# Performance work log

Measured on AMD Instinct MI355X. Metric: run time of the kernel, lower is better.

The kernel has to match this reference:

```python
import jax, jax.numpy as jnp
import numpy as np

N_NODES = 50000
N_EDGES = 800000
D = 128
K_HOPS = 2  # ConvLayer k=2 -> k+1=3 accumulated terms


def conv_layer(feat, src, dst, W, b):
    # DGL-style symmetric-norm GCN hop accumulation (method='sum', relu)
    n = feat.shape[0]
    ones = jnp.ones(src.shape[0], dtype=feat.dtype)
    deg = jax.ops.segment_sum(ones, src, num_segments=n)  # out-degrees
    norm = jnp.clip(deg, 1.0, None) ** -0.5  # [N]
    norm = norm[:, None]
    rst = feat @ W + b
    for _ in range(K_HOPS):
        feat = feat * norm
        # update_all(copy_u, sum): gather src features, scatter-sum to dst
        feat = jax.ops.segment_sum(feat[src], dst, num_segments=n)
        feat = feat * norm
        rst = rst + feat @ W + b  # original code reuses weights[0] each hop
    return jax.nn.relu(rst)


def setup_inputs() -> dict:
    key = jax.random.key(0)
    ks = jax.random.split(key, 6)
    xavier = (6.0 / (D + D)) ** 0.5
    feat = jax.random.normal(ks[0], (N_NODES, D), dtype=jnp.float32)
    src = jax.random.randint(ks[1], (N_EDGES,), 0, N_NODES, dtype=jnp.int32)
    dst = jax.random.randint(ks[2], (N_EDGES,), 0, N_NODES, dtype=jnp.int32)
    W1 = jax.random.uniform(ks[3], (D, D), jnp.float32, -xavier, xavier)
    W2 = jax.random.uniform(ks[4], (D, D), jnp.float32, -xavier, xavier)
    b1 = jnp.zeros((D,), jnp.float32)
    b2 = jnp.zeros((D,), jnp.float32)
    return {"feat": feat, "W1": W1, "b1": b1, "W2": W2, "b2": b2,
            "src": src, "dst": dst}


def reference(feat, W1, b1, W2, b2, src, dst):
    # GraphEmbbeding: stacked ConvLayers (num_layers=2)
    h = conv_layer(feat, src, dst, W1, b1)
    h = conv_layer(h, src, dst, W2, b2)
    return h
```

## Files before the change

### kernel.cpp

```cpp
#include <hip/hip_runtime.h>

#define N_NODES 50000
#define NP (N_NODES / 2)
#define N_EDGES 800000
#define D 128
#define NCH 128
#define EPC (N_EDGES / NCH)
#define NRB ((NP + 255) / 256)

typedef unsigned short ushort_t;
typedef unsigned int uint_t;
typedef short s16x8 __attribute__((ext_vector_type(8)));
typedef float f32x4 __attribute__((ext_vector_type(4)));

__device__ __forceinline__ float bf2f(ushort_t u) {
    uint_t x = ((uint_t)u) << 16;
    return __builtin_bit_cast(float, x);
}
__device__ __forceinline__ ushort_t f2bf(float f) {
    uint_t u = __builtin_bit_cast(uint_t, f);
    uint_t r = (u + 0x7FFFu + ((u >> 16) & 1u)) >> 16;
    return (ushort_t)r;
}

__global__ __launch_bounds__(256) void kb_hist(const int* __restrict__ src,
        const int* __restrict__ dst, uint_t* __restrict__ dhist,
        uint_t* __restrict__ shist) {
    __shared__ uint_t h[NP];
    int chunk = blockIdx.x;
    const int* arr = blockIdx.y ? src : dst;
    uint_t* out = (blockIdx.y ? shist : dhist) + (size_t)chunk * NP;
    int t = threadIdx.x;
    for (int i = t; i < NP; i += 256) h[i] = 0;
    __syncthreads();
    int e0 = chunk * EPC;
    for (int e = e0 + t; e < e0 + EPC; e += 256) {
        int n = arr[e];
        atomicAdd(&h[n >> 1], 1u << ((n & 1) * 16));
    }
    __syncthreads();
    for (int i = t; i < NP; i += 256) out[i] = h[i];
}

__global__ __launch_bounds__(256) void kb_reduce(uint_t* __restrict__ dhist,
        const uint_t* __restrict__ shist,
        int* __restrict__ off, int* __restrict__ bsum,
        float* __restrict__ norm, float* __restrict__ rnorm) {
    __shared__ int sh[256];
    int t = threadIdx.x;
    int p = blockIdx.x * 256 + t;
    int run0 = 0, run1 = 0, od0 = 0, od1 = 0;
    if (p < NP) {
#pragma unroll 8
        for (int c = 0; c < NCH; ++c) {
            size_t idx = (size_t)c * NP + p;
            uint_t v = dhist[idx];
            dhist[idx] = (uint_t)(run0 | (run1 << 16));
            run0 += (int)(v & 0xFFFFu);
            run1 += (int)(v >> 16);
            uint_t s = shist[idx];
            od0 += (int)(s & 0xFFFFu);
            od1 += (int)(s >> 16);
        }
        float dg0 = fmaxf((float)od0, 1.0f);
        float dg1 = fmaxf((float)od1, 1.0f);
        norm[2 * p]      = 1.0f / sqrtf(dg0);
        rnorm[2 * p]     = sqrtf(dg0);
        norm[2 * p + 1]  = 1.0f / sqrtf(dg1);
        rnorm[2 * p + 1] = sqrtf(dg1);
    }
    int tot = run0 + run1;
    sh[t] = tot;
    __syncthreads();
    for (int d = 1; d < 256; d <<= 1) {
        int x = sh[t];
        int y = (t >= d) ? sh[t - d] : 0;
        __syncthreads();
        sh[t] = x + y;
        __syncthreads();
    }
    if (p < NP) {
        int base = sh[t] - tot;
        off[2 * p]     = base;
        off[2 * p + 1] = base + run0;
    }
    if (t == 255) bsum[blockIdx.x] = sh[255];
}

__global__ void k_scanB(const int* __restrict__ bsum, int* __restrict__ bbase,
                        int* __restrict__ off) {
    __shared__ int sh[256];
    int t = threadIdx.x;
    int v = (t < NRB) ? bsum[t] : 0;
    sh[t] = v;
    __syncthreads();
    for (int d = 1; d < 256; d <<= 1) {
        int x = sh[t];
        int y = (t >= d) ? sh[t - d] : 0;
        __syncthreads();
        sh[t] = x + y;
        __syncthreads();
    }
    if (t < NRB) bbase[t] = sh[t] - v;
    if (t == 255) off[N_NODES] = sh[255];
}

__global__ void k_scanC(int* __restrict__ off, const int* __restrict__ bbase) {
    int i = blockIdx.x * 256 + threadIdx.x;
    if (i < N_NODES) off[i] += bbase[i >> 9];
}

__global__ __launch_bounds__(256) void kb_scatter(const int* __restrict__ src,
        const int* __restrict__ dst, const int* __restrict__ off,
        const uint_t* __restrict__ dhist, int* __restrict__ csrc) {
    __shared__ int slot[NP];
    int chunk = blockIdx.x, range = blockIdx.y;
    int base = range * NP;
    int t = threadIdx.x;
    const uint_t* hb = dhist + (size_t)chunk * NP + range * (NP / 2);
    for (int i = t; i < NP; i += 256) {
        uint_t cb = hb[i >> 1];
        int c16 = (int)((cb >> ((i & 1) * 16)) & 0xFFFFu);
        slot[i] = off[base + i] + c16;
    }
    __syncthreads();
    int e0 = chunk * EPC;
    for (int e = e0 + t; e < e0 + EPC; e += 256) {
        unsigned du = (unsigned)(dst[e] - base);
        if (du < (unsigned)NP) {
            int p = atomicAdd(&slot[du], 1);
            csrc[p] = src[e];
        }
    }
}

__global__ void k_prepw(const float* __restrict__ W1, const float* __restrict__ W2,
                        ushort_t* __restrict__ Wt1, ushort_t* __restrict__ Wt2) {
    int i = blockIdx.x * 256 + threadIdx.x;
    const float* W = blockIdx.y ? W2 : W1;
    ushort_t* Wt = blockIdx.y ? Wt2 : Wt1;
    if (i < D * D) {
        int col = i >> 7, k = i & 127;
        Wt[i] = f2bf(W[(size_t)k * D + col]);
    }
}

__global__ void k_init(const float* __restrict__ X, const float* __restrict__ norm,
                       ushort_t* __restrict__ A) {
    int i = blockIdx.x * blockDim.x + threadIdx.x;
    const int total = N_NODES * (D / 4);
    if (i < total) {
        int row = i >> 5;
        float4 v = ((const float4*)X)[i];
        float nm = norm[row];
        ushort4 a = {f2bf(v.x * nm), f2bf(v.y * nm), f2bf(v.z * nm), f2bf(v.w * nm)};
        ((ushort4*)A)[i] = a;
    }
}

__global__ __launch_bounds__(256, 2) void k_prop(const ushort_t* __restrict__ Ain,
                       const int* __restrict__ off, const int* __restrict__ csrc,
                       const float* __restrict__ norm,
                       ushort_t* __restrict__ Aout, int mode) {
    int w = blockIdx.x * 16 + (threadIdx.x >> 4);
    if (w >= N_NODES) return;
    int li = threadIdx.x & 15;
    int s0 = off[w], s1 = off[w + 1];
    float a0=0.f,a1=0.f,a2=0.f,a3=0.f,a4=0.f,a5=0.f,a6=0.f,a7=0.f;
    const s16x8* A8 = (const s16x8*)Ain;
    int j = s0;
    for (; j + 16 <= s1; j += 16) {
        int idx[16];
#pragma unroll
        for (int k = 0; k < 16; ++k) idx[k] = csrc[j + k];
        s16x8 v[16];
#pragma unroll
        for (int k = 0; k < 16; ++k) v[k] = A8[(size_t)idx[k] * 16 + li];
#pragma unroll
        for (int k = 0; k < 16; ++k) {
            a0 += bf2f((ushort_t)v[k][0]); a1 += bf2f((ushort_t)v[k][1]);
            a2 += bf2f((ushort_t)v[k][2]); a3 += bf2f((ushort_t)v[k][3]);
            a4 += bf2f((ushort_t)v[k][4]); a5 += bf2f((ushort_t)v[k][5]);
            a6 += bf2f((ushort_t)v[k][6]); a7 += bf2f((ushort_t)v[k][7]);
        }
    }
    if (j < s1) {
        int e1 = s1 - 1;
        for (; j < s1; j += 8) {
            int idx[8]; float wk[8];
#pragma unroll
            for (int k = 0; k < 8; ++k) {
                int jj = j + k;
                idx[k] = csrc[jj < s1 ? jj : e1];
                wk[k] = (jj < s1) ? 1.f : 0.f;
            }
            s16x8 v[8];
#pragma unroll
            for (int k = 0; k < 8; ++k) v[k] = A8[(size_t)idx[k] * 16 + li];
#pragma unroll
            for (int k = 0; k < 8; ++k) {
                a0 = fmaf(wk[k], bf2f((ushort_t)v[k][0]), a0);
                a1 = fmaf(wk[k], bf2f((ushort_t)v[k][1]), a1);
                a2 = fmaf(wk[k], bf2f((ushort_t)v[k][2]), a2);
                a3 = fmaf(wk[k], bf2f((ushort_t)v[k][3]), a3);
                a4 = fmaf(wk[k], bf2f((ushort_t)v[k][4]), a4);
                a5 = fmaf(wk[k], bf2f((ushort_t)v[k][5]), a5);
                a6 = fmaf(wk[k], bf2f((ushort_t)v[k][6]), a6);
                a7 = fmaf(wk[k], bf2f((ushort_t)v[k][7]), a7);
            }
        }
    }
    float nm = norm[w];
    float f = mode ? nm : nm * nm;
    s16x8 o;
    o[0] = (short)f2bf(a0 * f); o[1] = (short)f2bf(a1 * f);
    o[2] = (short)f2bf(a2 * f); o[3] = (short)f2bf(a3 * f);
    o[4] = (short)f2bf(a4 * f); o[5] = (short)f2bf(a5 * f);
    o[6] = (short)f2bf(a6 * f); o[7] = (short)f2bf(a7 * f);
    ((s16x8*)Aout)[(size_t)w * 16 + li] = o;
}

__global__ __launch_bounds__(256) void k_gemm_relu(const float* __restrict__ X0f,
        const ushort_t* __restrict__ X0h,
        const ushort_t* __restrict__ A1, const ushort_t* __restrict__ X2,
        const float* __restrict__ rnorm,
        const ushort_t* __restrict__ Wt, const float* __restrict__ bias,
        float* __restrict__ outf, ushort_t* __restrict__ Hbf,
        ushort_t* __restrict__ Anext,
        const float* __restrict__ norm, float bscale) {
    __shared__ ushort_t Xs[64 * D];
    __shared__ ushort_t Ws[D * D];
    int t = threadIdx.x;
    int row0 = blockIdx.x * 64;
    const s16x8* Wg = (const s16x8*)Wt;
    s16x8* Ws8 = (s16x8*)Ws;
    for (int i = t; i < D * 16; i += 256) {
        int col = i >> 4, c = i & 15;
        Ws8[(col << 4) | (c ^ (col & 7))] = Wg[i];
    }
    s16x8* Xs8 = (s16x8*)Xs;
    for (int i = t; i < 64 * 16; i += 256) {
        int r = i >> 4, c = i & 15;
        int gr = row0 + r;
        s16x8 ov;
        if (gr < N_NODES) {
            size_t b4 = (size_t)gr * 32 + c * 2;
            float x[8];
            if (X0f) {
                float4 x0a = ((const float4*)X0f)[b4], x0b = ((const float4*)X0f)[b4 + 1];
                x[0]=x0a.x; x[1]=x0a.y; x[2]=x0a.z; x[3]=x0a.w;
                x[4]=x0b.x; x[5]=x0b.y; x[6]=x0b.z; x[7]=x0b.w;
            } else {
                ushort4 h0 = ((const ushort4*)X0h)[b4], h1 = ((const ushort4*)X0h)[b4 + 1];
                x[0]=bf2f(h0.x); x[1]=bf2f(h0.y); x[2]=bf2f(h0.z); x[3]=bf2f(h0.w);
                x[4]=bf2f(h1.x); x[5]=bf2f(h1.y); x[6]=bf2f(h1.z); x[7]=bf2f(h1.w);
            }
            ushort4 p0 = ((const ushort4*)A1)[b4], p1 = ((const ushort4*)A1)[b4 + 1];
            ushort4 q0 = ((const ushort4*)X2)[b4], q1 = ((const ushort4*)X2)[b4 + 1];
            float rn = rnorm[gr];
            ov[0] = (short)f2bf(x[0] + bf2f(p0.x) * rn + bf2f(q0.x));
            ov[1] = (short)f2bf(x[1] + bf2f(p0.y) * rn + bf2f(q0.y));
            ov[2] = (short)f2bf(x[2] + bf2f(p0.z) * rn + bf2f(q0.z));
            ov[3] = (short)f2bf(x[3] + bf2f(p0.w) * rn + bf2f(q0.w));
            ov[4] = (short)f2bf(x[4] + bf2f(p1.x) * rn + bf2f(q1.x));
            ov[5] = (short)f2bf(x[5] + bf2f(p1.y) * rn + bf2f(q1.y));
            ov[6] = (short)f2bf(x[6] + bf2f(p1.z) * rn + bf2f(q1.z));
            ov[7] = (short)f2bf(x[7] + bf2f(p1.w) * rn + bf2f(q1.w));
        } else {
            ov = (s16x8)0;
        }
        Xs8[(r << 4) | (c ^ (r & 7))] = ov;
    }
    __syncthreads();
    int wid = t >> 6, l = t & 63;
    int lrow = l & 15, lk = l >> 4;
    f32x4 acc[8];
#pragma unroll
    for (int nt = 0; nt < 8; ++nt) acc[nt] = (f32x4){0.f, 0.f, 0.f, 0.f};
    const s16x8* Xr = (const s16x8*)Xs;
    const s16x8* Wr = (const s16x8*)Ws;
#pragma unroll
    for (int ks = 0; ks < 4; ++ks) {
        int kc = ks * 4 + lk;
        int ar = wid * 16 + lrow;
        s16x8 a = Xr[(ar << 4) | (kc ^ (ar & 7))];
#pragma unroll
        for (int nt = 0; nt < 8; ++nt) {
            int bc = nt * 16 + lrow;
            s16x8 b = Wr[(bc << 4) | (kc ^ (bc & 7))];
            acc[nt] = __builtin_amdgcn_mfma_f32_16x16x32_bf16(a, b, acc[nt], 0, 0, 0);
        }
    }
    int rbase = row0 + wid * 16 + lk * 4;
#pragma unroll
    for (int nt = 0; nt < 8; ++nt) {
        int C = nt * 16 + lrow;
        float bv = bias[C] * bscale;
#pragma unroll
        for (int r = 0; r < 4; ++r) {
            int R = rbase + r;
            if (R < N_NODES) {
                float o = fmaxf(acc[nt][r] + bv, 0.f);
                size_t oi = (size_t)R * D + C;
                if (outf) outf[oi] = o;
                if (Hbf) Hbf[oi] = f2bf(o);
                if (Anext) Anext[oi] = f2bf(o * norm[R]);
            }
        }
    }
}

extern "C" void kernel_launch(void* const* d_in, const int* in_sizes, int n_in,
                              void* d_out, int out_size, void* d_ws, size_t ws_size,
                              hipStream_t stream) {
    const float* feat = (const float*)d_in[0];
    const float* W1   = (const float*)d_in[1];
    const float* b1   = (const float*)d_in[2];
    const float* W2   = (const float*)d_in[3];
    const float* b2   = (const float*)d_in[4];
    const int*   src  = (const int*)d_in[5];
    const int*   dst  = (const int*)d_in[6];
    float* out = (float*)d_out;

    char* ws = (char*)d_ws;
    size_t o = 0;
    auto alloc = [&](size_t bytes) {
        void* p = ws + o;
        o += (bytes + 1023) & ~(size_t)1023;
        return p;
    };
    uint_t*   dhist = (uint_t*)alloc((size_t)NCH * NP * 4);
    uint_t*   shist = (uint_t*)alloc((size_t)NCH * NP * 4);
    float*    norm  = (float*)alloc(N_NODES * 4);
    float*    rnorm = (float*)alloc(N_NODES * 4);
    int*      off   = (int*)alloc((N_NODES + 1) * 4);
    int*      bsum  = (int*)alloc(NRB * 4);
    int*      bbase = (int*)alloc(NRB * 4);
    int*      csrc  = (int*)alloc((size_t)N_EDGES * 4);
    ushort_t* bufA  = (ushort_t*)alloc((size_t)N_NODES * D * 2);
    ushort_t* bufB  = (ushort_t*)alloc((size_t)N_NODES * D * 2);
    ushort_t* bufC  = (ushort_t*)alloc((size_t)N_NODES * D * 2);
    ushort_t* bufD  = (ushort_t*)alloc((size_t)N_NODES * D * 2);
    ushort_t* Wt1   = (ushort_t*)alloc((size_t)D * D * 2);
    ushort_t* Wt2   = (ushort_t*)alloc((size_t)D * D * 2);
    (void)ws_size; (void)in_sizes; (void)n_in; (void)out_size;

    kb_hist<<<dim3(NCH, 2), 256, 0, stream>>>(src, dst, dhist, shist);
    kb_reduce<<<NRB, 256, 0, stream>>>(dhist, shist, off, bsum, norm, rnorm);
    k_scanB<<<1, 256, 0, stream>>>(bsum, bbase, off);
    k_scanC<<<(N_NODES + 255) / 256, 256, 0, stream>>>(off, bbase);
    kb_scatter<<<dim3(NCH, 2), 256, 0, stream>>>(src, dst, off, dhist, csrc);
    k_prepw<<<dim3((D * D + 255) / 256, 2), 256, 0, stream>>>(W1, W2, Wt1, Wt2);

    const int init_blocks = (N_NODES * 32 + 255) / 256;
    const int prop_blocks = (N_NODES + 15) / 16;
    const int gemm_blocks = (N_NODES + 63) / 64;

    k_init<<<init_blocks, 256, 0, stream>>>(feat, norm, bufA);
    k_prop<<<prop_blocks, 256, 0, stream>>>(bufA, off, csrc, norm, bufB, 0);
    k_prop<<<prop_blocks, 256, 0, stream>>>(bufB, off, csrc, norm, bufC, 1);
    k_gemm_relu<<<gemm_blocks, 256, 0, stream>>>(feat, nullptr, bufB, bufC, rnorm,
                                                 Wt1, b1, nullptr, bufD, bufA, norm, 3.0f);

    k_prop<<<prop_blocks, 256, 0, stream>>>(bufA, off, csrc, norm, bufB, 0);
    k_prop<<<prop_blocks, 256, 0, stream>>>(bufB, off, csrc, norm, bufC, 1);
    k_gemm_relu<<<gemm_blocks, 256, 0, stream>>>(nullptr, bufD, bufB, bufC, rnorm,
                                                 Wt2, b2, out, nullptr, nullptr, norm, 3.0f);
}
```

Baseline: 229.5 us.

## Fuse setup kernels to cut launches and prefetch next CSR indices in propagation

Folds the weight transpose/convert into extra blocks of the histogram kernel, and merges the block-sum scan, offset fixup and feature init into one kernel where every block redundantly rescans the block sums. This removes three kernel launches and their serialization gaps. In the propagation kernel it prefetches the next 16 neighbour indices while the current feature gathers are in flight, so index loads overlap the gathers. The cost is redundant per-block scan work and higher register pressure in the gather loop.

```diff
diff --git a/kernel.cpp b/kernel.cpp
--- a/kernel.cpp
+++ b/kernel.cpp
@@ -7,6 +7,8 @@
 #define NCH 128
 #define EPC (N_EDGES / NCH)
 #define NRB ((NP + 255) / 256)
+#define SCB ((N_NODES + 255) / 256)
+#define INB ((N_NODES * (D / 4) + 255) / 256)
 
 typedef unsigned short ushort_t;
 typedef unsigned int uint_t;
@@ -25,8 +27,19 @@
 
 __global__ __launch_bounds__(256) void kb_hist(const int* __restrict__ src,
         const int* __restrict__ dst, uint_t* __restrict__ dhist,
-        uint_t* __restrict__ shist) {
+        uint_t* __restrict__ shist,
+        const float* __restrict__ W1, const float* __restrict__ W2,
+        ushort_t* __restrict__ Wt1, ushort_t* __restrict__ Wt2) {
     __shared__ uint_t h[NP];
+    if (blockIdx.y == 2) {
+        int x = blockIdx.x;
+        const float* W = (x & 64) ? W2 : W1;
+        ushort_t* Wt = (x & 64) ? Wt2 : Wt1;
+        int i = (x & 63) * 256 + threadIdx.x;
+        int col = i >> 7, k = i & 127;
+        Wt[i] = f2bf(W[(size_t)k * D + col]);
+        return;
+    }
     int chunk = blockIdx.x;
     const int* arr = blockIdx.y ? src : dst;
     uint_t* out = (blockIdx.y ? shist : dhist) + (size_t)chunk * NP;
@@ -87,27 +100,46 @@
     if (t == 255) bsum[blockIdx.x] = sh[255];
 }
 
-__global__ void k_scanB(const int* __restrict__ bsum, int* __restrict__ bbase,
-                        int* __restrict__ off) {
-    __shared__ int sh[256];
-    int t = threadIdx.x;
-    int v = (t < NRB) ? bsum[t] : 0;
-    sh[t] = v;
-    __syncthreads();
-    for (int d = 1; d < 256; d <<= 1) {
-        int x = sh[t];
-        int y = (t >= d) ? sh[t - d] : 0;
+__global__ __launch_bounds__(256) void k_scanC_init(int* __restrict__ off,
+        const int* __restrict__ bsum,
+        const float* __restrict__ X, const float* __restrict__ norm,
+        ushort_t* __restrict__ A) {
+    int b = blockIdx.x;
+    int t = threadIdx.x;
+    if (b < SCB) {
+        __shared__ int sh[128];
+        sh[t & 127] = (t < NRB) ? bsum[t] : 0;
         __syncthreads();
-        sh[t] = x + y;
+        if (t < 128) {
+            int v = (t < NRB) ? bsum[t] : 0;
+            sh[t] = v;
+        }
         __syncthreads();
-    }
-    if (t < NRB) bbase[t] = sh[t] - v;
-    if (t == 255) off[N_NODES] = sh[255];
-}
-
-__global__ void k_scanC(int* __restrict__ off, const int* __restrict__ bbase) {
-    int i = blockIdx.x * 256 + threadIdx.x;
-    if (i < N_NODES) off[i] += bbase[i >> 9];
+        for (int d = 1; d < 128; d <<= 1) {
+            int x = (t < 128) ? sh[t] : 0;
+            int y = (t >= d && t < 128) ? sh[t - d] : 0;
+            __syncthreads();
+            if (t < 128) sh[t] = x + y;
+            __syncthreads();
+        }
+        int i = b * 256 + t;
+        if (i < N_NODES) {
+            int rb = i >> 9;
+            int base = (rb > 0) ? sh[rb - 1] : 0;
+            off[i] += base;
+        }
+        if (b == 0 && t == 0) off[N_NODES] = sh[NRB - 1];
+    } else {
+        int i = (b - SCB) * 256 + t;
+        const int total = N_NODES * (D / 4);
+        if (i < total) {
+            int row = i >> 5;
+            float4 v = ((const float4*)X)[i];
+            float nm = norm[row];
+            ushort4 a = {f2bf(v.x * nm), f2bf(v.y * nm), f2bf(v.z * nm), f2bf(v.w * nm)};
+            ((ushort4*)A)[i] = a;
+        }
+    }
 }
 
 __global__ __launch_bounds__(256) void kb_scatter(const int* __restrict__ src,
@@ -131,30 +163,6 @@
             int p = atomicAdd(&slot[du], 1);
             csrc[p] = src[e];
         }
-    }
-}
-
-__global__ void k_prepw(const float* __restrict__ W1, const float* __restrict__ W2,
-                        ushort_t* __restrict__ Wt1, ushort_t* __restrict__ Wt2) {
-    int i = blockIdx.x * 256 + threadIdx.x;
-    const float* W = blockIdx.y ? W2 : W1;
-    ushort_t* Wt = blockIdx.y ? Wt2 : Wt1;
-    if (i < D * D) {
-        int col = i >> 7, k = i & 127;
-        Wt[i] = f2bf(W[(size_t)k * D + col]);
-    }
-}
-
-__global__ void k_init(const float* __restrict__ X, const float* __restrict__ norm,
-                       ushort_t* __restrict__ A) {
-    int i = blockIdx.x * blockDim.x + threadIdx.x;
-    const int total = N_NODES * (D / 4);
-    if (i < total) {
-        int row = i >> 5;
-        float4 v = ((const float4*)X)[i];
-        float nm = norm[row];
-        ushort4 a = {f2bf(v.x * nm), f2bf(v.y * nm), f2bf(v.z * nm), f2bf(v.w * nm)};
-        ((ushort4*)A)[i] = a;
     }
 }
 
@@ -168,14 +176,21 @@
     int s0 = off[w], s1 = off[w + 1];
     float a0=0.f,a1=0.f,a2=0.f,a3=0.f,a4=0.f,a5=0.f,a6=0.f,a7=0.f;
     const s16x8* A8 = (const s16x8*)Ain;
-    int j = s0;
-    for (; j + 16 <= s1; j += 16) {
-        int idx[16];
-#pragma unroll
-        for (int k = 0; k < 16; ++k) idx[k] = csrc[j + k];
+    int jend = s0 + ((s1 - s0) & ~15);
+    int idxA[16];
+    if (jend > s0) {
+#pragma unroll
+        for (int k = 0; k < 16; ++k) idxA[k] = csrc[s0 + k];
+    }
+    for (int j = s0; j < jend; j += 16) {
         s16x8 v[16];
 #pragma unroll
-        for (int k = 0; k < 16; ++k) v[k] = A8[(size_t)idx[k] * 16 + li];
+        for (int k = 0; k < 16; ++k) v[k] = A8[(size_t)idxA[k] * 16 + li];
+        int jn = j + 16;
+        if (jn < jend) {
+#pragma unroll
+            for (int k = 0; k < 16; ++k) idxA[k] = csrc[jn + k];
+        }
 #pragma unroll
         for (int k = 0; k < 16; ++k) {
             a0 += bf2f((ushort_t)v[k][0]); a1 += bf2f((ushort_t)v[k][1]);
@@ -184,9 +199,9 @@
             a6 += bf2f((ushort_t)v[k][6]); a7 += bf2f((ushort_t)v[k][7]);
         }
     }
-    if (j < s1) {
+    if (jend < s1) {
         int e1 = s1 - 1;
-        for (; j < s1; j += 8) {
+        for (int j = jend; j < s1; j += 8) {
             int idx[8]; float wk[8];
 #pragma unroll
             for (int k = 0; k < 8; ++k) {
@@ -335,7 +350,6 @@
     float*    rnorm = (float*)alloc(N_NODES * 4);
     int*      off   = (int*)alloc((N_NODES + 1) * 4);
     int*      bsum  = (int*)alloc(NRB * 4);
-    int*      bbase = (int*)alloc(NRB * 4);
     int*      csrc  = (int*)alloc((size_t)N_EDGES * 4);
     ushort_t* bufA  = (ushort_t*)alloc((size_t)N_NODES * D * 2);
     ushort_t* bufB  = (ushort_t*)alloc((size_t)N_NODES * D * 2);
@@ -345,18 +359,14 @@
     ushort_t* Wt2   = (ushort_t*)alloc((size_t)D * D * 2);
     (void)ws_size; (void)in_sizes; (void)n_in; (void)out_size;
 
-    kb_hist<<<dim3(NCH, 2), 256, 0, stream>>>(src, dst, dhist, shist);
+    kb_hist<<<dim3(NCH, 3), 256, 0, stream>>>(src, dst, dhist, shist, W1, W2, Wt1, Wt2);
     kb_reduce<<<NRB, 256, 0, stream>>>(dhist, shist, off, bsum, norm, rnorm);
-    k_scanB<<<1, 256, 0, stream>>>(bsum, bbase, off);
-    k_scanC<<<(N_NODES + 255) / 256, 256, 0, stream>>>(off, bbase);
+    k_scanC_init<<<SCB + INB, 256, 0, stream>>>(off, bsum, feat, norm, bufA);
     kb_scatter<<<dim3(NCH, 2), 256, 0, stream>>>(src, dst, off, dhist, csrc);
-    k_prepw<<<dim3((D * D + 255) / 256, 2), 256, 0, stream>>>(W1, W2, Wt1, Wt2);
-
-    const int init_blocks = (N_NODES * 32 + 255) / 256;
+
     const int prop_blocks = (N_NODES + 15) / 16;
     const int gemm_blocks = (N_NODES + 63) / 64;
 
-    k_init<<<init_blocks, 256, 0, stream>>>(feat, norm, bufA);
     k_prop<<<prop_blocks, 256, 0, stream>>>(bufA, off, csrc, norm, bufB, 0);
     k_prop<<<prop_blocks, 256, 0, stream>>>(bufB, off, csrc, norm, bufC, 1);
     k_gemm_relu<<<gemm_blocks, 256, 0, stream>>>(feat, nullptr, bufB, bufC, rnorm,
```

Result: slower. 236.9 us (+3.2%).
